# Kernel optimization log

Measured on AMD Instinct MI355X. Metric: run time of the kernel, lower is better.

Reference implementation:

```python
import jax, jax.numpy as jnp
import numpy as np

B, N, M, D = 4, 2048, 4096, 1
C, K = 4, 32
POINTS_PER_UNIT = 20


def setup_inputs() -> dict:
    key = jax.random.key(0)
    k1, k2, k3 = jax.random.split(key, 3)
    xz = jax.random.uniform(k1, (M, D), dtype=jnp.float32) * 4.0 - 2.0  # grid locations
    x = jax.random.uniform(k2, (B, N, D), dtype=jnp.float32) * 4.0 - 2.0  # target locations
    z = jax.random.normal(k3, (B, C, M, K), dtype=jnp.float32)
    log_scale = jnp.array([np.log(2.0 / POINTS_PER_UNIT)], dtype=jnp.float32)
    return {"xz": xz, "x": x, "z": z, "log_scale": log_scale}


def reference(xz, x, z, log_scale):
    # pairwise squared distances between grid xz [M,D] and targets x [B,N,D] -> [B,M,N]
    d2 = jnp.sum((xz[None, :, None, :] - x[:, None, :, :]) ** 2, axis=-1)
    # RBF weights (note: divided by exp(log_scale), matching original code)
    w = jnp.exp(-0.5 * d2 / jnp.exp(log_scale[0]))  # [B,M,N]
    # weights^T @ z with channel broadcast: [B,C,N,K]
    zt = jnp.einsum('bmn,bcmk->bcnk', w, z)
    # outer product z @ z^T: [B,C,N,N] positive semi-definite
    out = jnp.einsum('bcnk,bcmk->bcnm', zt, zt)
    return (xz, out)
```

## Files before the change

### kernel.cpp

```cpp
#include <hip/hip_runtime.h>
#include <hip/hip_bf16.h>

#define B_  4
#define N_  2048
#define M_  4096
#define C_  4
#define K_  32
#define CK_ 128

typedef float f32x4 __attribute__((ext_vector_type(4)));
typedef short s16x8 __attribute__((ext_vector_type(8)));

__device__ __forceinline__ short f2bf(float f) {
    union { __hip_bfloat16 h; short s; } u;
    u.h = __float2bfloat16(f);
    return u.s;
}
__device__ __forceinline__ float bf2f(unsigned short u) {
    return __uint_as_float((unsigned)u << 16);
}

__global__ __launch_bounds__(256) void z2bft_kernel(
    const float* __restrict__ z, unsigned short* __restrict__ zbt)
{
    __shared__ float t_f[K_][136];
    const int tid = threadIdx.x;
    const int m0  = blockIdx.x * 128;
    const int bc  = blockIdx.y;

    #pragma unroll
    for (int it = 0; it < 4; ++it) {
        const int e = tid + it * 256;
        const int m = e >> 3, k4 = e & 7;
        const f32x4 v = *(const f32x4*)&z[((size_t)bc * M_ + m0 + m) * K_ + k4 * 4];
        #pragma unroll
        for (int j = 0; j < 4; ++j) t_f[k4 * 4 + j][m] = v[j];
    }
    __syncthreads();
    #pragma unroll
    for (int it = 0; it < 2; ++it) {
        const int e = tid + it * 256;
        const int r = e >> 4, mq = e & 15;
        s16x8 pk;
        #pragma unroll
        for (int j = 0; j < 8; ++j) pk[j] = f2bf(t_f[r][mq * 8 + j]);
        *(s16x8*)&zbt[((size_t)(bc * K_ + r)) * M_ + m0 + mq * 8] = pk;
    }
}

#define ZS 136

template <int MS>
__global__ __launch_bounds__(512, 4) void zt_mfma_kernel(
    const float* __restrict__ xz, const float* __restrict__ x,
    const unsigned short* __restrict__ zbt, const float* __restrict__ ls,
    unsigned short* __restrict__ ztp)
{
    constexpr int MCH = M_ / MS;
    constexpr int NCH = MCH / 128;
    __shared__ __align__(16) float xz_s[MCH];
    __shared__ __align__(16) short z_s[2][CK_][ZS];

    const int tid  = threadIdx.x;
    const int lane = tid & 63;
    const int w    = tid >> 6;
    const int wq   = w >> 1;
    const int wc   = w & 1;
    const int l15  = lane & 15;
    const int lg   = lane >> 4;
    const int ms   = blockIdx.x;
    const int nblk = blockIdx.y * 128;
    const int b    = blockIdx.z;

    const float coef = -0.5f * __expf(-ls[0]);

    float xv[2];
    #pragma unroll
    for (int fa = 0; fa < 2; ++fa)
        xv[fa] = x[b * N_ + nblk + wq * 32 + fa * 16 + l15];

    const int mstart = ms * MCH;
    for (int i = tid; i < MCH; i += 512) xz_s[i] = xz[mstart + i];

    f32x4 acc[2][4];
    #pragma unroll
    for (int i = 0; i < 2; ++i)
        #pragma unroll
        for (int j = 0; j < 4; ++j) acc[i][j] = (f32x4)0.0f;

    s16x8 stg[4];
    #define LOADC(t) { _Pragma("unroll")                                          \
        for (int it = 0; it < 4; ++it) {                                          \
            const int u = tid + it * 512;                                         \
            const int ck = u >> 4, mq = u & 15;                                   \
            stg[it] = *(const s16x8*)&zbt[((size_t)(b * CK_ + ck)) * M_ +         \
                                          mstart + (t) * 128 + mq * 8];           \
        } }
    #define WRITEC(t) { _Pragma("unroll")                                         \
        for (int it = 0; it < 4; ++it) {                                          \
            const int u = tid + it * 512;                                         \
            const int ck = u >> 4, mq = u & 15;                                   \
            *(s16x8*)&z_s[(t) & 1][ck][mq * 8] = stg[it];                         \
        } }

    LOADC(0); WRITEC(0);
    __syncthreads();

    for (int t = 0; t < NCH; ++t) {
        if (t + 1 < NCH) LOADC(t + 1);
        #pragma unroll
        for (int ks = 0; ks < 4; ++ks) {
            const float* xzp = &xz_s[t * 128 + ks * 32 + lg * 8];
            const f32x4 t0 = *reinterpret_cast<const f32x4*>(xzp);
            const f32x4 t1 = *reinterpret_cast<const f32x4*>(xzp + 4);
            const float tt[8] = {t0.x, t0.y, t0.z, t0.w, t1.x, t1.y, t1.z, t1.w};
            s16x8 af[2];
            #pragma unroll
            for (int fa = 0; fa < 2; ++fa) {
                #pragma unroll
                for (int j = 0; j < 8; ++j) {
                    const float d = tt[j] - xv[fa];
                    af[fa][j] = f2bf(__expf(coef * d * d));
                }
            }
            s16x8 bfg[4];
            #pragma unroll
            for (int fc = 0; fc < 4; ++fc)
                bfg[fc] = *reinterpret_cast<const s16x8*>(
                    &z_s[t & 1][wc * 64 + fc * 16 + l15][ks * 32 + lg * 8]);
            #pragma unroll
            for (int fa = 0; fa < 2; ++fa)
                #pragma unroll
                for (int fc = 0; fc < 4; ++fc)
                    acc[fa][fc] = __builtin_amdgcn_mfma_f32_16x16x32_bf16(
                        af[fa], bfg[fc], acc[fa][fc], 0, 0, 0);
        }
        if (t + 1 < NCH) WRITEC(t + 1);
        __syncthreads();
    }

    unsigned short* dst = ztp + (size_t)ms * (B_ * C_ * N_ * K_);
    #pragma unroll
    for (int fc = 0; fc < 4; ++fc) {
        const int ck = wc * 64 + fc * 16 + l15;
        const int c  = ck >> 5, k = ck & 31;
        #pragma unroll
        for (int fa = 0; fa < 2; ++fa) {
            const int n0 = nblk + wq * 32 + fa * 16 + lg * 4;
            #pragma unroll
            for (int r = 0; r < 4; ++r)
                dst[(((size_t)b * C_ + c) * N_ + n0 + r) * K_ + k] =
                    (unsigned short)f2bf(acc[fa][fc][r]);
        }
    }
    #undef LOADC
    #undef WRITEC
}

template <int MS>
__global__ __launch_bounds__(256) void zt_reduce_copy_kernel(
    const unsigned short* __restrict__ ztp, unsigned short* __restrict__ ztb,
    const float* __restrict__ xz, float* __restrict__ out)
{
    if (blockIdx.x >= 1024) {
        const int t = (blockIdx.x - 1024) * 256 + threadIdx.x;
        *(float4*)&out[t * 4] = *(const float4*)&xz[t * 4];
        return;
    }
    const size_t t      = (size_t)blockIdx.x * 256 + threadIdx.x;
    const size_t stride = (size_t)(B_ * C_ * N_ * K_);
    float s0 = 0.f, s1 = 0.f, s2 = 0.f, s3 = 0.f;
    #pragma unroll
    for (int p = 0; p < MS; ++p) {
        const ushort4 v = *(const ushort4*)&ztp[(size_t)p * stride + t * 4];
        s0 += bf2f(v.x); s1 += bf2f(v.y); s2 += bf2f(v.z); s3 += bf2f(v.w);
    }
    ushort4 pk;
    pk.x = (unsigned short)f2bf(s0); pk.y = (unsigned short)f2bf(s1);
    pk.z = (unsigned short)f2bf(s2); pk.w = (unsigned short)f2bf(s3);
    *(ushort4*)&ztb[t * 4] = pk;
}

#define TB 128
__global__ __launch_bounds__(256, 4) void out_mfma_kernel(
    const unsigned short* __restrict__ ztb, float* __restrict__ out)
{
    __shared__ __align__(16) float t_s[64][132];

    const int tid  = threadIdx.x;
    const int lane = tid & 63;
    const int wave = tid >> 6;
    const int wn   = wave >> 1;
    const int wm   = wave & 1;
    const int l15  = lane & 15;
    const int lg   = lane >> 4;
    const int mblk = blockIdx.x * TB;
    const int nblk = blockIdx.y * TB;
    const int bc   = blockIdx.z;

    const unsigned short* base = ztb + (size_t)bc * (N_ * K_);

    s16x8 afr[4], bfr[4];
    #pragma unroll
    for (int f = 0; f < 4; ++f) {
        const int n = nblk + wn * 64 + f * 16 + l15;
        afr[f] = *reinterpret_cast<const s16x8*>(&base[(size_t)n * K_ + lg * 8]);
        const int m = mblk + wm * 64 + f * 16 + l15;
        bfr[f] = *reinterpret_cast<const s16x8*>(&base[(size_t)m * K_ + lg * 8]);
    }

    f32x4 acc[4][4];
    #pragma unroll
    for (int i = 0; i < 4; ++i)
        #pragma unroll
        for (int j = 0; j < 4; ++j) acc[i][j] = (f32x4)0.0f;

    #pragma unroll
    for (int fa = 0; fa < 4; ++fa)
        #pragma unroll
        for (int fm = 0; fm < 4; ++fm)
            acc[fa][fm] = __builtin_amdgcn_mfma_f32_16x16x32_bf16(
                afr[fa], bfr[fm], acc[fa][fm], 0, 0, 0);

    float* ob = out + (size_t)bc * N_ * N_;

    #pragma unroll
    for (int p = 0; p < 2; ++p) {
        if (p) __syncthreads();
        if (wn == p) {
            #pragma unroll
            for (int fa = 0; fa < 4; ++fa) {
                const int row0 = fa * 16 + lg * 4;
                #pragma unroll
                for (int fm = 0; fm < 4; ++fm) {
                    const int mcol = wm * 64 + fm * 16 + l15;
                    #pragma unroll
                    for (int r = 0; r < 4; ++r)
                        t_s[row0 + r][mcol] = acc[fa][fm][r];
                }
            }
        }
        __syncthreads();
        #pragma unroll
        for (int it = 0; it < 8; ++it) {
            const int e   = tid + it * 256;
            const int row = e >> 5;
            const int c4  = e & 31;
            const f32x4 v = *reinterpret_cast<const f32x4*>(&t_s[row][c4 * 4]);
            __builtin_nontemporal_store(
                v, (f32x4*)&ob[(size_t)(nblk + p * 64 + row) * N_ + mblk + c4 * 4]);
        }
    }
}

extern "C" void kernel_launch(void* const* d_in, const int* in_sizes, int n_in,
                              void* d_out, int out_size, void* d_ws, size_t ws_size,
                              hipStream_t stream)
{
    const float* xz = (const float*)d_in[0];
    const float* x  = (const float*)d_in[1];
    const float* z  = (const float*)d_in[2];
    const float* ls = (const float*)d_in[3];
    float* out = (float*)d_out;

    (void)in_sizes; (void)n_in; (void)out_size;

    const size_t ztf = (size_t)B_ * C_ * N_ * K_;
    unsigned short* ztb = (unsigned short*)d_ws;
    unsigned short* zbt = ztb + ztf;
    unsigned short* ztp = zbt + (size_t)B_ * CK_ * M_;

    z2bft_kernel<<<dim3(M_ / 128, B_ * C_), dim3(256), 0, stream>>>(z, zbt);

    const size_t base_b = ztf * 2 + (size_t)B_ * CK_ * M_ * 2;
    if (ws_size >= base_b + (size_t)8 * ztf * 2) {
        zt_mfma_kernel<8><<<dim3(8, N_ / 128, B_), dim3(512), 0, stream>>>(xz, x, zbt, ls, ztp);
        zt_reduce_copy_kernel<8><<<dim3(1028), dim3(256), 0, stream>>>(ztp, ztb, xz, out);
    } else if (ws_size >= base_b + (size_t)4 * ztf * 2) {
        zt_mfma_kernel<4><<<dim3(4, N_ / 128, B_), dim3(512), 0, stream>>>(xz, x, zbt, ls, ztp);
        zt_reduce_copy_kernel<4><<<dim3(1028), dim3(256), 0, stream>>>(ztp, ztb, xz, out);
    } else {
        zt_mfma_kernel<2><<<dim3(2, N_ / 128, B_), dim3(512), 0, stream>>>(xz, x, zbt, ls, ztp);
        zt_reduce_copy_kernel<2><<<dim3(1028), dim3(256), 0, stream>>>(ztp, ztb, xz, out);
    }

    out_mfma_kernel<<<dim3(N_ / TB, N_ / TB, B_ * C_), dim3(256), 0, stream>>>(ztb, out + M_);
}
```

Before: 82.16 us.

## Pre-swizzle z into MFMA fragment layout and load B operands directly from global

The z preprocessing kernel now writes bf16 z in the exact per-lane MFMA B-fragment order. The main zt kernel drops its double-buffered LDS staging and per-tile barriers, and instead register-prefetches the next fragment straight from global memory. This is meant to remove LDS traffic and synchronisation in the inner loop, at the cost of more scattered strided reads in the conversion kernel and exposed global load latency. The output kernel's nontemporal stores are also replaced with ordinary stores.

```diff
diff --git a/kernel.cpp b/kernel.cpp
--- a/kernel.cpp
+++ b/kernel.cpp
@@ -1,12 +1,13 @@
 #include <hip/hip_runtime.h>
 #include <hip/hip_bf16.h>
 
-#define B_  4
-#define N_  2048
-#define M_  4096
-#define C_  4
-#define K_  32
-#define CK_ 128
+#define B_   4
+#define N_   2048
+#define M_   4096
+#define C_   4
+#define K_   32
+#define CK_  128
+#define M32_ (M_ / 32)
 
 typedef float f32x4 __attribute__((ext_vector_type(4)));
 typedef short s16x8 __attribute__((ext_vector_type(8)));
@@ -20,46 +21,35 @@
     return __uint_as_float((unsigned)u << 16);
 }
 
-__global__ __launch_bounds__(256) void z2bft_kernel(
-    const float* __restrict__ z, unsigned short* __restrict__ zbt)
-{
-    __shared__ float t_f[K_][136];
-    const int tid = threadIdx.x;
-    const int m0  = blockIdx.x * 128;
-    const int bc  = blockIdx.y;
-
-    #pragma unroll
-    for (int it = 0; it < 4; ++it) {
-        const int e = tid + it * 256;
-        const int m = e >> 3, k4 = e & 7;
-        const f32x4 v = *(const f32x4*)&z[((size_t)bc * M_ + m0 + m) * K_ + k4 * 4];
-        #pragma unroll
-        for (int j = 0; j < 4; ++j) t_f[k4 * 4 + j][m] = v[j];
-    }
-    __syncthreads();
-    #pragma unroll
-    for (int it = 0; it < 2; ++it) {
-        const int e = tid + it * 256;
-        const int r = e >> 4, mq = e & 15;
-        s16x8 pk;
-        #pragma unroll
-        for (int j = 0; j < 8; ++j) pk[j] = f2bf(t_f[r][mq * 8 + j]);
-        *(s16x8*)&zbt[((size_t)(bc * K_ + r)) * M_ + m0 + mq * 8] = pk;
-    }
-}
-
-#define ZS 136
+__global__ __launch_bounds__(256) void z2frag_kernel(
+    const float* __restrict__ z, unsigned short* __restrict__ zf)
+{
+    const unsigned u = blockIdx.x * 256 + threadIdx.x;
+    const int s   = u & 63;
+    const int lg  = s >> 4, l15 = s & 15;
+    const int m32 = (u >> 6) & (M32_ - 1);
+    const int g   = (u >> 13) & 7;
+    const int b   = u >> 16;
+    const int c   = g >> 1;
+    const int k   = (g & 1) * 16 + l15;
+    const int m0  = m32 * 32 + lg * 8;
+
+    const float* src = &z[(((size_t)(b * C_ + c)) * M_ + m0) * K_ + k];
+    s16x8 pk;
+    #pragma unroll
+    for (int e = 0; e < 8; ++e) pk[e] = f2bf(src[(size_t)e * K_]);
+    *(s16x8*)&zf[(size_t)u * 8] = pk;
+}
 
 template <int MS>
 __global__ __launch_bounds__(512, 4) void zt_mfma_kernel(
     const float* __restrict__ xz, const float* __restrict__ x,
-    const unsigned short* __restrict__ zbt, const float* __restrict__ ls,
+    const unsigned short* __restrict__ zf, const float* __restrict__ ls,
     unsigned short* __restrict__ ztp)
 {
     constexpr int MCH = M_ / MS;
-    constexpr int NCH = MCH / 128;
+    constexpr int L   = MCH / 32;
     __shared__ __align__(16) float xz_s[MCH];
-    __shared__ __align__(16) short z_s[2][CK_][ZS];
 
     const int tid  = threadIdx.x;
     const int lane = tid & 63;
@@ -81,6 +71,7 @@
 
     const int mstart = ms * MCH;
     for (int i = tid; i < MCH; i += 512) xz_s[i] = xz[mstart + i];
+    __syncthreads();
 
     f32x4 acc[2][4];
     #pragma unroll
@@ -88,55 +79,43 @@
         #pragma unroll
         for (int j = 0; j < 4; ++j) acc[i][j] = (f32x4)0.0f;
 
-    s16x8 stg[4];
-    #define LOADC(t) { _Pragma("unroll")                                          \
-        for (int it = 0; it < 4; ++it) {                                          \
-            const int u = tid + it * 512;                                         \
-            const int ck = u >> 4, mq = u & 15;                                   \
-            stg[it] = *(const s16x8*)&zbt[((size_t)(b * CK_ + ck)) * M_ +         \
-                                          mstart + (t) * 128 + mq * 8];           \
-        } }
-    #define WRITEC(t) { _Pragma("unroll")                                         \
-        for (int it = 0; it < 4; ++it) {                                          \
-            const int u = tid + it * 512;                                         \
-            const int ck = u >> 4, mq = u & 15;                                   \
-            *(s16x8*)&z_s[(t) & 1][ck][mq * 8] = stg[it];                         \
-        } }
-
-    LOADC(0); WRITEC(0);
-    __syncthreads();
-
-    for (int t = 0; t < NCH; ++t) {
-        if (t + 1 < NCH) LOADC(t + 1);
-        #pragma unroll
-        for (int ks = 0; ks < 4; ++ks) {
-            const float* xzp = &xz_s[t * 128 + ks * 32 + lg * 8];
-            const f32x4 t0 = *reinterpret_cast<const f32x4*>(xzp);
-            const f32x4 t1 = *reinterpret_cast<const f32x4*>(xzp + 4);
-            const float tt[8] = {t0.x, t0.y, t0.z, t0.w, t1.x, t1.y, t1.z, t1.w};
-            s16x8 af[2];
-            #pragma unroll
-            for (int fa = 0; fa < 2; ++fa) {
-                #pragma unroll
-                for (int j = 0; j < 8; ++j) {
-                    const float d = tt[j] - xv[fa];
-                    af[fa][j] = f2bf(__expf(coef * d * d));
-                }
+    const unsigned short* fbase =
+        &zf[(((size_t)(b * 8 + wc * 4)) * M32_ + mstart / 32) * 512 + lane * 8];
+
+    s16x8 nb[4];
+    #pragma unroll
+    for (int fc = 0; fc < 4; ++fc)
+        nb[fc] = *(const s16x8*)&fbase[(size_t)fc * M32_ * 512];
+
+    #pragma unroll 4
+    for (int ms32 = 0; ms32 < L; ++ms32) {
+        s16x8 cb[4];
+        #pragma unroll
+        for (int fc = 0; fc < 4; ++fc) cb[fc] = nb[fc];
+        if (ms32 + 1 < L) {
+            #pragma unroll
+            for (int fc = 0; fc < 4; ++fc)
+                nb[fc] = *(const s16x8*)&fbase[((size_t)fc * M32_ + ms32 + 1) * 512];
+        }
+        const float* xzp = &xz_s[ms32 * 32 + lg * 8];
+        const f32x4 t0 = *reinterpret_cast<const f32x4*>(xzp);
+        const f32x4 t1 = *reinterpret_cast<const f32x4*>(xzp + 4);
+        const float tt[8] = {t0.x, t0.y, t0.z, t0.w, t1.x, t1.y, t1.z, t1.w};
+        s16x8 af[2];
+        #pragma unroll
+        for (int fa = 0; fa < 2; ++fa) {
+            #pragma unroll
+            for (int j = 0; j < 8; ++j) {
+                const float d = tt[j] - xv[fa];
+                af[fa][j] = f2bf(__expf(coef * d * d));
             }
-            s16x8 bfg[4];
+        }
+        #pragma unroll
+        for (int fa = 0; fa < 2; ++fa)
             #pragma unroll
             for (int fc = 0; fc < 4; ++fc)
-                bfg[fc] = *reinterpret_cast<const s16x8*>(
-                    &z_s[t & 1][wc * 64 + fc * 16 + l15][ks * 32 + lg * 8]);
-            #pragma unroll
-            for (int fa = 0; fa < 2; ++fa)
-                #pragma unroll
-                for (int fc = 0; fc < 4; ++fc)
-                    acc[fa][fc] = __builtin_amdgcn_mfma_f32_16x16x32_bf16(
-                        af[fa], bfg[fc], acc[fa][fc], 0, 0, 0);
-        }
-        if (t + 1 < NCH) WRITEC(t + 1);
-        __syncthreads();
+                acc[fa][fc] = __builtin_amdgcn_mfma_f32_16x16x32_bf16(
+                    af[fa], cb[fc], acc[fa][fc], 0, 0, 0);
     }
 
     unsigned short* dst = ztp + (size_t)ms * (B_ * C_ * N_ * K_);
@@ -153,8 +132,6 @@
                     (unsigned short)f2bf(acc[fa][fc][r]);
         }
     }
-    #undef LOADC
-    #undef WRITEC
 }
 
 template <int MS>
@@ -247,8 +224,7 @@
             const int row = e >> 5;
             const int c4  = e & 31;
             const f32x4 v = *reinterpret_cast<const f32x4*>(&t_s[row][c4 * 4]);
-            __builtin_nontemporal_store(
-                v, (f32x4*)&ob[(size_t)(nblk + p * 64 + row) * N_ + mblk + c4 * 4]);
+            *(f32x4*)&ob[(size_t)(nblk + p * 64 + row) * N_ + mblk + c4 * 4] = v;
         }
     }
 }
@@ -267,20 +243,20 @@
 
     const size_t ztf = (size_t)B_ * C_ * N_ * K_;
     unsigned short* ztb = (unsigned short*)d_ws;
-    unsigned short* zbt = ztb + ztf;
-    unsigned short* ztp = zbt + (size_t)B_ * CK_ * M_;
-
-    z2bft_kernel<<<dim3(M_ / 128, B_ * C_), dim3(256), 0, stream>>>(z, zbt);
+    unsigned short* zf  = ztb + ztf;
+    unsigned short* ztp = zf + (size_t)B_ * CK_ * M_;
+
+    z2frag_kernel<<<dim3((unsigned)(B_ * 8 * M32_ * 64 / 256)), dim3(256), 0, stream>>>(z, zf);
 
     const size_t base_b = ztf * 2 + (size_t)B_ * CK_ * M_ * 2;
     if (ws_size >= base_b + (size_t)8 * ztf * 2) {
-        zt_mfma_kernel<8><<<dim3(8, N_ / 128, B_), dim3(512), 0, stream>>>(xz, x, zbt, ls, ztp);
+        zt_mfma_kernel<8><<<dim3(8, N_ / 128, B_), dim3(512), 0, stream>>>(xz, x, zf, ls, ztp);
         zt_reduce_copy_kernel<8><<<dim3(1028), dim3(256), 0, stream>>>(ztp, ztb, xz, out);
     } else if (ws_size >= base_b + (size_t)4 * ztf * 2) {
-        zt_mfma_kernel<4><<<dim3(4, N_ / 128, B_), dim3(512), 0, stream>>>(xz, x, zbt, ls, ztp);
+        zt_mfma_kernel<4><<<dim3(4, N_ / 128, B_), dim3(512), 0, stream>>>(xz, x, zf, ls, ztp);
         zt_reduce_copy_kernel<4><<<dim3(1028), dim3(256), 0, stream>>>(ztp, ztb, xz, out);
     } else {
-        zt_mfma_kernel<2><<<dim3(2, N_ / 128, B_), dim3(512), 0, stream>>>(xz, x, zbt, ls, ztp);
+        zt_mfma_kernel<2><<<dim3(2, N_ / 128, B_), dim3(512), 0, stream>>>(xz, x, zf, ls, ztp);
         zt_reduce_copy_kernel<2><<<dim3(1028), dim3(256), 0, stream>>>(ztp, ztb, xz, out);
     }
 
```

New measurement: 82.56 us. Within noise of the previous version (+0.5%).
